# Optimization experiments

Measured on AMD Instinct MI355X. Metric: run time of the kernel, lower is better.

## Reference

```python
import jax, jax.numpy as jnp
import numpy as np

NUM_HEADS = 12

def get_rel_pos(q_size, k_size, rel_pos):
    # q_size == k_size here; relative index = i - j + (k_size - 1)
    idx = jnp.arange(q_size)[:, None] - jnp.arange(k_size)[None, :] + (k_size - 1)
    return rel_pos[idx]  # (q_size, k_size, head_dim)


def setup_inputs() -> dict:
    key = jax.random.key(0)
    ks = jax.random.split(key, 7)
    B, H, W, C = 1, 64, 64, 768
    return {
        "x": jax.random.normal(ks[0], (B, H, W, C), jnp.float32),
        "w_qkv": jax.random.normal(ks[1], (C, 3 * C), jnp.float32) * 0.02,
        "b_qkv": jnp.zeros((3 * C,), jnp.float32),
        "w_o": jax.random.normal(ks[2], (C, C), jnp.float32) * 0.02,
        "b_o": jnp.zeros((C,), jnp.float32),
        "rel_pos_h": jax.random.normal(ks[3], (2 * H - 1, C // NUM_HEADS), jnp.float32) * 0.02,
        "rel_pos_w": jax.random.normal(ks[4], (2 * W - 1, C // NUM_HEADS), jnp.float32) * 0.02,
    }


def reference(x, w_qkv, b_qkv, w_o, b_o, rel_pos_h, rel_pos_w):
    B, H, W, C = x.shape
    NH = NUM_HEADS
    HD = C // NH
    scale = HD ** -0.5  # 0.125

    qkv = x @ w_qkv + b_qkv                                   # (B,H,W,3C)
    qkv = qkv.reshape(B, H * W, 3, NH, HD)
    qkv = jnp.transpose(qkv, (2, 0, 3, 1, 4)).reshape(3, B * NH, H * W, HD)
    q, k, v = qkv[0], qkv[1], qkv[2]                          # (B*NH, HW, HD)

    Rh = get_rel_pos(H, H, rel_pos_h)                         # (H,H,HD)
    Rw = get_rel_pos(W, W, rel_pos_w)                         # (W,W,HD)
    qr = q.reshape(B * NH, H, W, HD)
    rel_h = jnp.einsum('bhwc,hkc->bhwk', qr, Rh)              # (B*NH,H,W,H)
    rel_w = jnp.einsum('bhwc,wkc->bhwk', qr, Rw)              # (B*NH,H,W,W)

    attn = jnp.einsum('bmd,bnd->bmn', q, k) * scale           # (B*NH,HW,HW)
    attn = attn.reshape(B * NH, H, W, H, W)
    attn = attn + rel_h[:, :, :, :, None] + rel_w[:, :, :, None, :]
    attn = attn.reshape(B * NH, H * W, H * W)

    p = jax.nn.softmax(attn, axis=-1)
    o = jnp.einsum('bmn,bnd->bmd', p, v)                      # (B*NH,HW,HD)
    o = o.reshape(B, NH, H * W, HD)
    o = jnp.transpose(o, (0, 2, 1, 3)).reshape(B, H, W, C)    # heads concat in channel dim
    return o @ w_o + b_o
```

## Files before the change

### kernel.cpp

```cpp
#include <hip/hip_runtime.h>

#define DEVI __device__ __forceinline__
typedef unsigned short u16;
typedef unsigned int u32;
typedef __attribute__((ext_vector_type(4))) float f4v;
typedef __attribute__((ext_vector_type(8))) short bf8v;
typedef __attribute__((ext_vector_type(4))) u32  u32x4;
typedef __attribute__((ext_vector_type(2))) u32  u32x2;
typedef __attribute__((ext_vector_type(4))) u16  u16x4;

#define AS1 __attribute__((address_space(1)))
#define AS3 __attribute__((address_space(3)))

DEVI u16 f2bf(float x){ union{float f;u32 u;} c{x}; u32 r=(c.u+0x7FFFu+((c.u>>16)&1u))>>16; return (u16)r; }
DEVI float bf2f(u16 b){ union{u32 u;float f;} c{(u32)b<<16}; return c.f; }
DEVI f4v mfma32(bf8v a, bf8v b, f4v c){ return __builtin_amdgcn_mfma_f32_16x16x32_bf16(a,b,c,0,0,0); }
DEVI unsigned lds_off(const void* p){ return (unsigned)(unsigned long)(AS3 const void*)p; }
DEVI void glds16(const void* g, void* l){
  __builtin_amdgcn_global_load_lds((AS1 void*)g, (AS3 void*)l, 16, 0, 0);
}

static constexpr int NH = 12, HW = 4096, D = 64, C = 768;
static constexpr float LOG2E = 1.44269504f;

__global__ void qa_prep(const float* __restrict__ x, u16* __restrict__ xb,
                        const float* __restrict__ wqkv, u16* __restrict__ wqkvt,
                        const float* __restrict__ wo,   u16* __restrict__ wot){
  __shared__ float tl[32][33];
  const int b = blockIdx.x, t = threadIdx.x;
  if(b < 3072){
    int i = b*256 + t;
    f4v v = ((const f4v*)x)[i];
    u16x4 o; for(int j=0;j<4;j++) o[j] = f2bf(v[j]);
    ((u16x4*)xb)[i] = o;
    return;
  }
  const float* in; u16* out; int R, Cc, scale_k, bx, by;
  if(b < 3072 + 1728){ int bb = b - 3072; in = wqkv; out = wqkvt; R = 768; Cc = 2304; scale_k = 1; bx = bb % 72; by = bb / 72; }
  else               { int bb = b - 4800; in = wo;   out = wot;   R = 768; Cc = 768;  scale_k = 0; bx = bb % 24; by = bb / 24; }
  int r0 = by*32, c0 = bx*32;
  int tr = t>>3, tc = (t&7)*4;
  f4v v = *(const f4v*)&in[(r0+tr)*Cc + c0 + tc];
  for(int j=0;j<4;j++) tl[tr][tc+j] = v[j];
  __syncthreads();
  int oc = t>>3, orr = (t&7)*4;
  float sc = (scale_k && (c0+oc) >= 768 && (c0+oc) < 1536) ? 0.125f*LOG2E : 1.0f;
  u16x4 o; for(int j=0;j<4;j++) o[j] = f2bf(tl[orr+j][oc]*sc);
  *(u16x4*)&out[(c0+oc)*R + r0 + orr] = o;
}

#define GEMM_STAGE(K0, BUF) \
  for(int i=0;i<2;i++){ \
    glds16(A  + (size_t)(m0+srow[i])*768 + (K0) + skk[i], (u16*)Al[BUF] + i*2048 + w*512); \
    glds16(Bt + (size_t)(n0+srow[i])*768 + (K0) + skk[i], (u16*)Bl[BUF] + i*2048 + w*512); }

#define GEMM_STEP(KIDX) { \
  if((KIDX) < 23) asm volatile("s_waitcnt vmcnt(4)\n\ts_barrier" ::: "memory"); \
  else            asm volatile("s_waitcnt vmcnt(0)\n\ts_barrier" ::: "memory"); \
  if((KIDX)+2 < 24) GEMM_STAGE(((KIDX)+2)*32, ((KIDX)+2)%3); \
  const int CUR=(KIDX)%3; \
  bf8v a[4], b[4]; \
  for(int mt=0;mt<4;mt++) a[mt] = *(const bf8v*)&Al[CUR][(wr*64+mt*16+c16)*32 + h4*8]; \
  for(int nt=0;nt<4;nt++) b[nt] = *(const bf8v*)&Bl[CUR][(wc*64+nt*16+c16)*32 + h4*8]; \
  __builtin_amdgcn_s_setprio(1); \
  for(int mt=0;mt<4;mt++) for(int nt=0;nt<4;nt++) acc[mt][nt] = mfma32(b[nt], a[mt], acc[mt][nt]); \
  __builtin_amdgcn_s_setprio(0); }

__global__ __launch_bounds__(256,2) void qa_gemm_qkv(
    const u16* __restrict__ A, const u16* __restrict__ Bt, const float* __restrict__ bias,
    u16* __restrict__ qb, u16* __restrict__ kb, u16* __restrict__ vb){
  __shared__ u16 Al[3][4096], Bl[3][4096];
  const int t = threadIdx.x, lane = t&63, w = t>>6, c16 = lane&15, h4 = lane>>4;
  const int m0 = blockIdx.y*128, n0 = blockIdx.x*128;
  const int wr = w>>1, wc = w&1;
  f4v acc[4][4];
  for(int nt=0;nt<4;nt++){
    f4v bv;
    for(int r=0;r<4;r++){
      int col = n0 + wc*64 + nt*16 + 4*h4 + r;
      float b = bias[col];
      bv[r] = (col >= 768 && col < 1536) ? b*0.125f*LOG2E : b;
    }
    for(int mt=0;mt<4;mt++) acc[mt][nt] = bv;
  }
  int srow[2], skk[2];
  for(int i=0;i<2;i++){
    int off = i*4096 + w*1024 + lane*16;
    srow[i] = off>>6; skk[i] = (off&63)>>1;
  }
  GEMM_STAGE(0, 0); GEMM_STAGE(32, 1);
  #pragma unroll
  for(int p=0;p<8;p++){ GEMM_STEP(3*p); GEMM_STEP(3*p+1); GEMM_STEP(3*p+2); }
  for(int mt=0;mt<4;mt++){
    int row = m0 + wr*64 + mt*16 + c16;
    for(int nt=0;nt<4;nt++){
      int col0 = n0 + wc*64 + nt*16 + 4*h4;
      int which = col0/768, head = (col0>>6)%12, d0 = col0&63;
      u16* dst = which==0 ? qb : (which==1 ? kb : vb);
      u32x2 pk;
      asm("v_cvt_pk_bf16_f32 %0, %1, %2" : "=v"(pk[0]) : "v"(acc[mt][nt][0]), "v"(acc[mt][nt][1]));
      asm("v_cvt_pk_bf16_f32 %0, %1, %2" : "=v"(pk[1]) : "v"(acc[mt][nt][2]), "v"(acc[mt][nt][3]));
      *(u32x2*)&dst[((size_t)(head<<12)+row)*64 + d0] = pk;
    }
  }
}

__global__ __launch_bounds__(256) void qa_rel(
    const u16* __restrict__ qbuf, const float* __restrict__ rph, const float* __restrict__ rpw,
    u16* __restrict__ RHt, u16* __restrict__ RW){
  const int t = threadIdx.x, lane = t&63, w = t>>6, c16 = lane&15, h4 = lane>>4;
  const int qh = blockIdx.x, head = blockIdx.y;
  __shared__ u16 ql[64*72], hl[64*72], wl[128*72];
  {
    int row = t>>2, d0 = (t&3)*16;
    const u16* src = qbuf + ((size_t)(head<<12)+(qh<<6)+row)*64 + d0;
    *(u32x4*)&ql[row*72+d0]   = *(const u32x4*)src;
    *(u32x4*)&ql[row*72+d0+8] = *(const u32x4*)(src+8);
    for(int j=0;j<16;j+=4){
      f4v v = *(const f4v*)&rph[(qh+row)*64 + d0 + j];
      u32x2 pk;
      asm("v_cvt_pk_bf16_f32 %0, %1, %2" : "=v"(pk[0]) : "v"(v[0]), "v"(v[1]));
      asm("v_cvt_pk_bf16_f32 %0, %1, %2" : "=v"(pk[1]) : "v"(v[2]), "v"(v[3]));
      *(u32x2*)&hl[row*72+d0+j] = pk;
    }
    int rw_r = t>>1, rd0 = (t&1)*32;
    if(rw_r < 127){
      for(int j=0;j<32;j+=4){
        f4v v = *(const f4v*)&rpw[rw_r*64+rd0+j];
        u32x2 pk;
        asm("v_cvt_pk_bf16_f32 %0, %1, %2" : "=v"(pk[0]) : "v"(v[0]), "v"(v[1]));
        asm("v_cvt_pk_bf16_f32 %0, %1, %2" : "=v"(pk[1]) : "v"(v[2]), "v"(v[3]));
        *(u32x2*)&wl[rw_r*72+rd0+j] = pk;
      }
    } else {
      for(int j=0;j<32;j+=4) *(u32x2*)&wl[rw_r*72+rd0+j] = (u32x2){0u,0u};
    }
  }
  __syncthreads();
  if(w < 2){
    bf8v a[2][2]; f4v acc[2][4] = {};
    for(int mt=0;mt<2;mt++) for(int ch=0;ch<2;ch++)
      a[mt][ch] = *(const bf8v*)&ql[(w*32+mt*16+c16)*72 + ch*32 + h4*8];
    for(int nt=0;nt<4;nt++) for(int ch=0;ch<2;ch++){
      bf8v b = *(const bf8v*)&hl[(nt*16+c16)*72 + ch*32 + h4*8];
      for(int mt=0;mt<2;mt++) acc[mt][nt] = mfma32(a[mt][ch], b, acc[mt][nt]);
    }
    for(int mt=0;mt<2;mt++) for(int nt=0;nt<4;nt++) for(int r=0;r<4;r++){
      int qw = w*32+mt*16+4*h4+r, c = nt*16+c16, kh = 63 - c;
      RHt[((size_t)(head*64+qh)*64+kh)*64 + qw] = f2bf(acc[mt][nt][r]*LOG2E);
    }
  } else {
    bf8v a[2][2]; f4v acc[2][8] = {};
    for(int mt=0;mt<2;mt++) for(int ch=0;ch<2;ch++)
      a[mt][ch] = *(const bf8v*)&ql[((w-2)*32+mt*16+c16)*72 + ch*32 + h4*8];
    for(int nt=0;nt<8;nt++) for(int ch=0;ch<2;ch++){
      bf8v b = *(const bf8v*)&wl[(nt*16+c16)*72 + ch*32 + h4*8];
      for(int mt=0;mt<2;mt++) acc[mt][nt] = mfma32(a[mt][ch], b, acc[mt][nt]);
    }
    for(int mt=0;mt<2;mt++) for(int nt=0;nt<8;nt++) for(int r=0;r<4;r++){
      int qw = (w-2)*32+mt*16+4*h4+r, c = nt*16+c16, kw = qw + 63 - c;
      if((unsigned)kw < 64u) RW[((size_t)(head*64+qh)*64+qw)*64 + kw] = f2bf(acc[mt][nt][r]*LOG2E);
    }
  }
}

#define AITER(IT, CUR) { \
    asm volatile("s_barrier" ::: "memory"); \
    if((IT) == 31){ kp = kg; vp = vg; } \
    { u16* Kn = (u16*)Kl[(CUR)^1]; u16* Vn = (u16*)Vl[(CUR)^1]; \
      for(int i=0;i<2;i++){ \
        glds16(kp + koff[i], Kn + (i*256 + w*64)*8); \
        glds16(vp + voff[i], Vn + (i*256 + w*64)*8); } } \
    kp += 4096; vp += 4096; \
    asm volatile("s_waitcnt vmcnt(4)" ::: "memory"); \
    const char* Kc = (const char*)Kl[CUR]; \
    float rh0 = bf2f(RHl[qhl*2048 + (IT)*64 + (w&1)*32 + c16]); \
    float rh1 = bf2f(RHl[qhl*2048 + (IT)*64 + (w&1)*32 + 16 + c16]); \
    f4v p[4][2]; \
    _Pragma("unroll") \
    for(int nt=0;nt<4;nt++){ \
      bf8v k0 = *(const bf8v*)(Kc + kA + nt*2048 + kq0); \
      bf8v k1 = *(const bf8v*)(Kc + kA + nt*2048 + kq1); \
      _Pragma("unroll") \
      for(int qc=0;qc<2;qc++){ \
        f4v sv; float rh = qc ? rh1 : rh0; \
        for(int r=0;r<4;r++) sv[r] = rh + rw[nt][qc][r]; \
        __builtin_amdgcn_s_setprio(1); \
        sv = mfma32(k0, qa[qc][0], sv); \
        sv = mfma32(k1, qa[qc][1], sv); \
        __builtin_amdgcn_s_setprio(0); \
        f4v pe; \
        for(int r=0;r<4;r++) pe[r] = __builtin_amdgcn_exp2f(sv[r]); \
        p[nt][qc] = pe; } } \
    union U8 { u32 wd[4]; bf8v v; }; \
    U8 pb[2][2]; \
    _Pragma("unroll") \
    for(int half=0;half<2;half++) \
      for(int qc=0;qc<2;qc++) \
        for(int i=0;i<4;i++){ \
          int nt = half*2 + (i>>1), r0 = (i&1)*2; \
          asm("v_cvt_pk_bf16_f32 %0, %1, %2" \
              : "=v"(pb[half][qc].wd[i]) : "v"(p[nt][qc][r0]), "v"(p[nt][qc][r0+1])); } \
    _Pragma("unroll") \
    for(int qc=0;qc<2;qc++){ \
      psacc[qc] = mfma32(onesv, pb[0][qc].v, psacc[qc]); \
      psacc[qc] = mfma32(onesv, pb[1][qc].v, psacc[qc]); } \
    unsigned vcur = vbase + (CUR)*8192; \
    _Pragma("unroll") \
    for(int dt=0;dt<4;dt++){ \
      unsigned long t00,t01,t10,t11; \
      asm volatile( \
        "ds_read_b64_tr_b16 %0, %4 offset:%c5\n\t" \
        "ds_read_b64_tr_b16 %1, %4 offset:%c6\n\t" \
        "ds_read_b64_tr_b16 %2, %4 offset:%c7\n\t" \
        "ds_read_b64_tr_b16 %3, %4 offset:%c8\n\t" \
        "s_waitcnt lgkmcnt(0)" \
        : "=&v"(t00), "=&v"(t01), "=&v"(t10), "=&v"(t11) \
        : "v"(vcur), "i"((dt)*2048), "i"((dt)*2048+512), "i"((dt)*2048+1024), "i"((dt)*2048+1536) \
        : "memory"); \
      union PV { struct{ unsigned long a,b; } q; bf8v v; }; \
      PV v01, v23; \
      v01.q.a = t00; v01.q.b = t01; v23.q.a = t10; v23.q.b = t11; \
      __builtin_amdgcn_s_setprio(1); \
      _Pragma("unroll") \
      for(int qc=0;qc<2;qc++){ \
        oacc[dt][qc] = mfma32(v01.v, pb[0][qc].v, oacc[dt][qc]); \
        oacc[dt][qc] = mfma32(v23.v, pb[1][qc].v, oacc[dt][qc]); } \
      __builtin_amdgcn_s_setprio(0); } \
  }

__global__ __launch_bounds__(256,3) void qa_attn(
    const u16* __restrict__ qb, const u16* __restrict__ kb, const u16* __restrict__ vb,
    const u16* __restrict__ RHt, const u16* __restrict__ RW,
    u16* __restrict__ Op, float* __restrict__ Ps){
  __shared__ u16 Kl[2][4096];
  __shared__ u16 Vl[2][4096];
  __shared__ u16 RHl[4096];
  const int t = threadIdx.x, lane = t&63, w = t>>6, c16 = lane&15, h4 = lane>>4;
  const int bid = blockIdx.x;
  const int g = (bid&7)*96 + (bid>>3);
  const int s = g&1, u = g>>1;
  const int head = u>>5, qblk = u&31;
  const int B0 = qblk*128;
  const int qhl = w>>1;

  for(int i=0;i<2;i++){
    const u16* rhsrc = RHt + (((size_t)(head*64 + qblk*2 + i))*64 + s*32)*64;
    glds16(rhsrc + t*8, (u16*)RHl + i*2048 + w*512);
  }
  int koff[2], voff[2];
  for(int i=0;i<2;i++){
    int uu = i*256 + t;
    koff[i] = (uu ^ ((uu>>3)&7))*8;
    int key = ((uu>>1)&3) | (((uu>>3)&15)<<2);
    int d0  = ((uu&1)<<3) | (((uu>>7)&3)<<4);
    voff[i] = key*64 + d0;
  }
  const u16* kg = kb + (size_t)head*262144 + (size_t)s*131072;
  const u16* vg = vb + (size_t)head*262144 + (size_t)s*131072;
  const u16* kp = kg; const u16* vp = vg;
  for(int i=0;i<2;i++){
    glds16(kp + koff[i], (u16*)Kl[0] + (i*256 + w*64)*8);
    glds16(vp + voff[i], (u16*)Vl[0] + (i*256 + w*64)*8);
  }
  kp += 4096; vp += 4096;

  bf8v qa[2][2];
  for(int qc=0;qc<2;qc++){
    const u16* qsrc = qb + ((size_t)head*4096 + B0 + w*32 + qc*16 + c16)*64;
    qa[qc][0] = *(const bf8v*)(qsrc + h4*8);
    qa[qc][1] = *(const bf8v*)(qsrc + 32 + h4*8);
  }
  float rw[4][2][4];
  for(int nt=0;nt<4;nt++) for(int qc=0;qc<2;qc++) for(int r=0;r<4;r++){
    int qw = (w&1)*32 + qc*16 + c16, kw = nt*16 + 4*h4 + r;
    rw[nt][qc][r] = bf2f(RW[(((size_t)(head*64 + qblk*2 + qhl))*64 + qw)*64 + kw]);
  }
  bf8v onesv; for(int j=0;j<8;j++) onesv[j] = (short)0x3F80;

  f4v oacc[4][2] = {}; f4v psacc[2] = {};
  const unsigned vbase = lds_off(Vl) + lane*8;
  const int kq0 = (h4*16) ^ ((c16&7)<<4);
  const int kq1 = (h4*16 + 64) ^ ((c16&7)<<4);
  const int kA  = c16*128;

  for(int itp=0; itp<16; itp++){
    AITER(2*itp, 0);
    AITER(2*itp+1, 1);
  }
  asm volatile("s_waitcnt vmcnt(0)" ::: "memory");

  #pragma unroll
  for(int qc=0;qc<2;qc++){
    float v = psacc[qc][0];
    const int qrow_l = w*32 + qc*16 + c16;
    if(h4 == 0) Ps[((size_t)u*2 + s)*128 + qrow_l] = v;
    const size_t obase = (((size_t)u*2 + s)*128 + qrow_l)*64;
    #pragma unroll
    for(int dt=0;dt<4;dt++){
      u32x2 pk;
      asm("v_cvt_pk_bf16_f32 %0, %1, %2" : "=v"(pk[0]) : "v"(oacc[dt][qc][0]), "v"(oacc[dt][qc][1]));
      asm("v_cvt_pk_bf16_f32 %0, %1, %2" : "=v"(pk[1]) : "v"(oacc[dt][qc][2]), "v"(oacc[dt][qc][3]));
      *(u32x2*)&Op[obase + dt*16 + 4*h4] = pk;
    }
  }
}

__global__ __launch_bounds__(256) void qa_reduce(
    const u16* __restrict__ Op, const float* __restrict__ Ps, u16* __restrict__ ob){
  const int u = blockIdx.x, t = threadIdx.x;
  const int head = u>>5, qblk = u&31;
  const int d0 = (t&15)*4;
  const size_t b0 = (size_t)u*2*128, b1 = b0 + 128;
  #pragma unroll
  for(int qq=0;qq<8;qq++){
    int qr = (t>>4) + qq*16;
    float inv = 1.0f / (Ps[b0 + qr] + Ps[b1 + qr]);
    u16x4 a = *(const u16x4*)&Op[(b0 + qr)*64 + d0];
    u16x4 b = *(const u16x4*)&Op[(b1 + qr)*64 + d0];
    u16x4 o;
    for(int j=0;j<4;j++) o[j] = f2bf((bf2f(a[j]) + bf2f(b[j]))*inv);
    *(u16x4*)&ob[(size_t)(qblk*128 + qr)*768 + head*64 + d0] = o;
  }
}

__global__ __launch_bounds__(256,2) void qa_gemm_out(
    const u16* __restrict__ A, const u16* __restrict__ Bt, const float* __restrict__ bias,
    float* __restrict__ out){
  __shared__ u16 Al[3][4096], Bl[3][4096];
  const int t = threadIdx.x, lane = t&63, w = t>>6, c16 = lane&15, h4 = lane>>4;
  const int m0 = blockIdx.y*128, n0 = blockIdx.x*128;
  const int wr = w>>1, wc = w&1;
  f4v acc[4][4];
  for(int nt=0;nt<4;nt++){
    f4v bv = *(const f4v*)&bias[n0 + wc*64 + nt*16 + 4*h4];
    for(int mt=0;mt<4;mt++) acc[mt][nt] = bv;
  }
  int srow[2], skk[2];
  for(int i=0;i<2;i++){
    int off = i*4096 + w*1024 + lane*16;
    srow[i] = off>>6; skk[i] = (off&63)>>1;
  }
  GEMM_STAGE(0, 0); GEMM_STAGE(32, 1);
  #pragma unroll
  for(int p=0;p<8;p++){ GEMM_STEP(3*p); GEMM_STEP(3*p+1); GEMM_STEP(3*p+2); }
  for(int mt=0;mt<4;mt++){
    int row = m0 + wr*64 + mt*16 + c16;
    for(int nt=0;nt<4;nt++){
      int col0 = n0 + wc*64 + nt*16 + 4*h4;
      *(f4v*)&out[(size_t)row*768 + col0] = acc[mt][nt];
    }
  }
}

extern "C" void kernel_launch(void* const* d_in, const int* in_sizes, int n_in,
                              void* d_out, int out_size, void* d_ws, size_t ws_size,
                              hipStream_t stream){
  const float* x    = (const float*)d_in[0];
  const float* wqkv = (const float*)d_in[1];
  const float* bqkv = (const float*)d_in[2];
  const float* wo   = (const float*)d_in[3];
  const float* bo   = (const float*)d_in[4];
  const float* rph  = (const float*)d_in[5];
  const float* rpw  = (const float*)d_in[6];
  float* out = (float*)d_out;

  size_t off = 0;
  auto alloc = [&](size_t bytes){ void* p = (char*)d_ws + off; off += (bytes + 255) & ~(size_t)255; return p; };
  u16* x_bf   = (u16*)alloc((size_t)HW*C*2);
  u16* wqkv_t = (u16*)alloc((size_t)2304*768*2);
  u16* wo_t   = (u16*)alloc((size_t)768*768*2);
  u16* q_buf  = (u16*)alloc((size_t)NH*HW*D*2);
  u16* k_buf  = (u16*)alloc((size_t)NH*HW*D*2);
  u16* v_buf  = (u16*)alloc((size_t)NH*HW*D*2);
  u16* rh_buf = (u16*)alloc((size_t)NH*64*64*64*2);
  u16* rw_buf = (u16*)alloc((size_t)NH*64*64*64*2);
  u16* o_buf  = (u16*)alloc((size_t)HW*C*2);
  u16* op_buf = (u16*)alloc((size_t)384*2*128*64*2);
  float* ps_buf = (float*)alloc((size_t)384*2*128*4);

  qa_prep<<<5376, 256, 0, stream>>>(x, x_bf, wqkv, wqkv_t, wo, wo_t);
  qa_gemm_qkv<<<dim3(2304/128, HW/128), 256, 0, stream>>>(x_bf, wqkv_t, bqkv, q_buf, k_buf, v_buf);
  qa_rel<<<dim3(64, NH), 256, 0, stream>>>(q_buf, rph, rpw, rh_buf, rw_buf);
  qa_attn<<<768, 256, 0, stream>>>(q_buf, k_buf, v_buf, rh_buf, rw_buf, op_buf, ps_buf);
  qa_reduce<<<384, 256, 0, stream>>>(op_buf, ps_buf, o_buf);
  qa_gemm_out<<<dim3(768/128, HW/128), 256, 0, stream>>>(o_buf, wo_t, bo, out);
}
```

Measured before the change: 132.9 us.

## Split attention KV range four ways and alias workspace buffers

The attention kernel now splits each query block's key range into four segments instead of two. That doubles the grid to 1536 blocks, halves the per-block iteration count and RH shared-memory footprint, and raises the launch-bounds occupancy hint to 4. The reduce kernel sums four partial outputs and denominators. Workspace buffers are laid out at fixed offsets with aliasing (op_buf over x_bf, o_buf over rh_buf) to shrink footprint and possibly improve cache locality, which depends on the lifetimes not overlapping. The split adds more partial-output traffic and reduction work in exchange for better load balance and occupancy across CUs.

```diff
diff --git a/kernel.cpp b/kernel.cpp
--- a/kernel.cpp
+++ b/kernel.cpp
@@ -166,7 +166,7 @@
 
 #define AITER(IT, CUR) { \
     asm volatile("s_barrier" ::: "memory"); \
-    if((IT) == 31){ kp = kg; vp = vg; } \
+    if((IT) == 15){ kp = kg; vp = vg; } \
     { u16* Kn = (u16*)Kl[(CUR)^1]; u16* Vn = (u16*)Vl[(CUR)^1]; \
       for(int i=0;i<2;i++){ \
         glds16(kp + koff[i], Kn + (i*256 + w*64)*8); \
@@ -174,8 +174,8 @@
     kp += 4096; vp += 4096; \
     asm volatile("s_waitcnt vmcnt(4)" ::: "memory"); \
     const char* Kc = (const char*)Kl[CUR]; \
-    float rh0 = bf2f(RHl[qhl*2048 + (IT)*64 + (w&1)*32 + c16]); \
-    float rh1 = bf2f(RHl[qhl*2048 + (IT)*64 + (w&1)*32 + 16 + c16]); \
+    float rh0 = bf2f(RHl[qhl][(IT)*64 + (w&1)*32 + c16]); \
+    float rh1 = bf2f(RHl[qhl][(IT)*64 + (w&1)*32 + 16 + c16]); \
     f4v p[4][2]; \
     _Pragma("unroll") \
     for(int nt=0;nt<4;nt++){ \
@@ -229,24 +229,24 @@
       __builtin_amdgcn_s_setprio(0); } \
   }
 
-__global__ __launch_bounds__(256,3) void qa_attn(
+__global__ __launch_bounds__(256,4) void qa_attn(
     const u16* __restrict__ qb, const u16* __restrict__ kb, const u16* __restrict__ vb,
     const u16* __restrict__ RHt, const u16* __restrict__ RW,
     u16* __restrict__ Op, float* __restrict__ Ps){
   __shared__ u16 Kl[2][4096];
   __shared__ u16 Vl[2][4096];
-  __shared__ u16 RHl[4096];
+  __shared__ u16 RHl[2][1024];
   const int t = threadIdx.x, lane = t&63, w = t>>6, c16 = lane&15, h4 = lane>>4;
   const int bid = blockIdx.x;
-  const int g = (bid&7)*96 + (bid>>3);
-  const int s = g&1, u = g>>1;
+  const int g = (bid&7)*192 + (bid>>3);
+  const int s = g&3, u = g>>2;
   const int head = u>>5, qblk = u&31;
   const int B0 = qblk*128;
   const int qhl = w>>1;
 
-  for(int i=0;i<2;i++){
-    const u16* rhsrc = RHt + (((size_t)(head*64 + qblk*2 + i))*64 + s*32)*64;
-    glds16(rhsrc + t*8, (u16*)RHl + i*2048 + w*512);
+  {
+    const u16* rhsrc = RHt + (((size_t)(head*64 + qblk*2 + qhl))*64 + s*16)*64;
+    glds16(rhsrc + (w&1)*512 + lane*8, (u16*)RHl[qhl] + (w&1)*512);
   }
   int koff[2], voff[2];
   for(int i=0;i<2;i++){
@@ -256,8 +256,8 @@
     int d0  = ((uu&1)<<3) | (((uu>>7)&3)<<4);
     voff[i] = key*64 + d0;
   }
-  const u16* kg = kb + (size_t)head*262144 + (size_t)s*131072;
-  const u16* vg = vb + (size_t)head*262144 + (size_t)s*131072;
+  const u16* kg = kb + (size_t)head*262144 + (size_t)s*65536;
+  const u16* vg = vb + (size_t)head*262144 + (size_t)s*65536;
   const u16* kp = kg; const u16* vp = vg;
   for(int i=0;i<2;i++){
     glds16(kp + koff[i], (u16*)Kl[0] + (i*256 + w*64)*8);
@@ -284,7 +284,7 @@
   const int kq1 = (h4*16 + 64) ^ ((c16&7)<<4);
   const int kA  = c16*128;
 
-  for(int itp=0; itp<16; itp++){
+  for(int itp=0; itp<8; itp++){
     AITER(2*itp, 0);
     AITER(2*itp+1, 1);
   }
@@ -294,8 +294,8 @@
   for(int qc=0;qc<2;qc++){
     float v = psacc[qc][0];
     const int qrow_l = w*32 + qc*16 + c16;
-    if(h4 == 0) Ps[((size_t)u*2 + s)*128 + qrow_l] = v;
-    const size_t obase = (((size_t)u*2 + s)*128 + qrow_l)*64;
+    if(h4 == 0) Ps[((size_t)u*4 + s)*128 + qrow_l] = v;
+    const size_t obase = (((size_t)u*4 + s)*128 + qrow_l)*64;
     #pragma unroll
     for(int dt=0;dt<4;dt++){
       u32x2 pk;
@@ -311,15 +311,22 @@
   const int u = blockIdx.x, t = threadIdx.x;
   const int head = u>>5, qblk = u&31;
   const int d0 = (t&15)*4;
-  const size_t b0 = (size_t)u*2*128, b1 = b0 + 128;
+  const size_t base = (size_t)u*4*128;
   #pragma unroll
   for(int qq=0;qq<8;qq++){
     int qr = (t>>4) + qq*16;
-    float inv = 1.0f / (Ps[b0 + qr] + Ps[b1 + qr]);
-    u16x4 a = *(const u16x4*)&Op[(b0 + qr)*64 + d0];
-    u16x4 b = *(const u16x4*)&Op[(b1 + qr)*64 + d0];
+    float tot = 0.f;
+    #pragma unroll
+    for(int s2=0;s2<4;s2++) tot += Ps[base + s2*128 + qr];
+    float inv = 1.0f/tot;
+    float a[4] = {0,0,0,0};
+    #pragma unroll
+    for(int s2=0;s2<4;s2++){
+      u16x4 v = *(const u16x4*)&Op[(base + s2*128 + qr)*64 + d0];
+      for(int j=0;j<4;j++) a[j] += bf2f(v[j]);
+    }
     u16x4 o;
-    for(int j=0;j<4;j++) o[j] = f2bf((bf2f(a[j]) + bf2f(b[j]))*inv);
+    for(int j=0;j<4;j++) o[j] = f2bf(a[j]*inv);
     *(u16x4*)&ob[(size_t)(qblk*128 + qr)*768 + head*64 + d0] = o;
   }
 }
@@ -365,24 +372,23 @@
   const float* rpw  = (const float*)d_in[6];
   float* out = (float*)d_out;
 
-  size_t off = 0;
-  auto alloc = [&](size_t bytes){ void* p = (char*)d_ws + off; off += (bytes + 255) & ~(size_t)255; return p; };
-  u16* x_bf   = (u16*)alloc((size_t)HW*C*2);
-  u16* wqkv_t = (u16*)alloc((size_t)2304*768*2);
-  u16* wo_t   = (u16*)alloc((size_t)768*768*2);
-  u16* q_buf  = (u16*)alloc((size_t)NH*HW*D*2);
-  u16* k_buf  = (u16*)alloc((size_t)NH*HW*D*2);
-  u16* v_buf  = (u16*)alloc((size_t)NH*HW*D*2);
-  u16* rh_buf = (u16*)alloc((size_t)NH*64*64*64*2);
-  u16* rw_buf = (u16*)alloc((size_t)NH*64*64*64*2);
-  u16* o_buf  = (u16*)alloc((size_t)HW*C*2);
-  u16* op_buf = (u16*)alloc((size_t)384*2*128*64*2);
-  float* ps_buf = (float*)alloc((size_t)384*2*128*4);
+  char* W = (char*)d_ws;
+  u16*   op_buf = (u16*)(W + 0);
+  u16*   x_bf   = (u16*)(W + 0);
+  u16*   wqkv_t = (u16*)(W + 6291456);
+  float* ps_buf = (float*)(W + 25165824);
+  u16*   wo_t   = (u16*)(W + 25952256);
+  u16*   q_buf  = (u16*)(W + 27131904);
+  u16*   k_buf  = (u16*)(W + 33423360);
+  u16*   v_buf  = (u16*)(W + 39714816);
+  u16*   rh_buf = (u16*)(W + 46006272);
+  u16*   o_buf  = (u16*)(W + 46006272);
+  u16*   rw_buf = (u16*)(W + 52297728);
 
   qa_prep<<<5376, 256, 0, stream>>>(x, x_bf, wqkv, wqkv_t, wo, wo_t);
   qa_gemm_qkv<<<dim3(2304/128, HW/128), 256, 0, stream>>>(x_bf, wqkv_t, bqkv, q_buf, k_buf, v_buf);
   qa_rel<<<dim3(64, NH), 256, 0, stream>>>(q_buf, rph, rpw, rh_buf, rw_buf);
-  qa_attn<<<768, 256, 0, stream>>>(q_buf, k_buf, v_buf, rh_buf, rw_buf, op_buf, ps_buf);
+  qa_attn<<<1536, 256, 0, stream>>>(q_buf, k_buf, v_buf, rh_buf, rw_buf, op_buf, ps_buf);
   qa_reduce<<<384, 256, 0, stream>>>(op_buf, ps_buf, o_buf);
   qa_gemm_out<<<dim3(768/128, HW/128), 256, 0, stream>>>(o_buf, wo_t, bo, out);
 }
```

Measured after the change: 240.8 us. 81.2% more time.
